# Performance work log

Hardware: AMD Instinct MI355X
Metric: run time of the kernel (lower is better)

The kernel has to match this reference:

```python
import jax, jax.numpy as jnp
import numpy as np


def setup_inputs() -> dict:
    key = jax.random.key(0)
    evecs = jax.random.normal(key, (4, 1, 1024, 16), dtype=jnp.float32)
    return {"evecs": evecs}


def reference(evecs):
    # Original wraps everything in torch.set_grad_enabled(False) -> block grads.
    evecs = jax.lax.stop_gradient(evecs)
    B, C, N, K = evecs.shape
    # For each level lvl, the torch loop computes X[..., :lvl+1] @ X[..., :lvl+1]^T,
    # i.e. the cumulative sum over k of rank-1 outer products e_k e_k^T.
    # outers[b, k, c, n, m] = evecs[b, c, n, k] * evecs[b, c, m, k]
    outers = jnp.einsum('bcnk,bcmk->bkcnm', evecs, evecs)
    cube = jnp.cumsum(outers, axis=1)          # running low-rank approximations
    # torch.cat(lras, dim=1): level-major then channel -> [B, K*C, N, N]
    return cube.reshape(B, K * C, N, N)
```

## Files before the change

kernel.cpp:

```cpp
#include <hip/hip_runtime.h>


#define BB 4
#define NN 1024
#define KK 16
#define ROWS 8

__global__ __launch_bounds__(256) void ExpandEvecs_75780402970966_kernel(
    const float* __restrict__ ev,
    float* __restrict__ out)
{
    const int tid = threadIdx.x;
    const int m0  = tid << 2;
    const int grp = blockIdx.x & 127;
    const int b   = blockIdx.x >> 7;
    const int n0  = grp * ROWS;

    const float* eb = ev + (size_t)b * NN * KK;

    float acc[ROWS][4];
#pragma unroll
    for (int r = 0; r < ROWS; ++r)
#pragma unroll
        for (int v = 0; v < 4; ++v) acc[r][v] = 0.0f;

    const size_t kplane = (size_t)NN * NN;
    const size_t obase  = (size_t)b * KK * kplane + (size_t)n0 * NN + (size_t)m0;

#pragma unroll
    for (int kb = 0; kb < KK / 4; ++kb) {
        float4 em4[4];
#pragma unroll
        for (int v = 0; v < 4; ++v)
            em4[v] = *(const float4*)(eb + (size_t)(m0 + v) * KK + kb * 4);

        float4 en4[ROWS];
#pragma unroll
        for (int r = 0; r < ROWS; ++r)
            en4[r] = *(const float4*)(eb + (size_t)(n0 + r) * KK + kb * 4);

#pragma unroll
        for (int kk = 0; kk < 4; ++kk) {
            const int k = kb * 4 + kk;
            float* outk = out + obase + (size_t)k * kplane;
#pragma unroll
            for (int r = 0; r < ROWS; ++r) {
                const float enk = ((const float*)&en4[r])[kk];
#pragma unroll
                for (int v = 0; v < 4; ++v)
                    acc[r][v] = fmaf(((const float*)&em4[v])[kk], enk, acc[r][v]);
                *(float4*)(outk + (size_t)r * NN) =
                    make_float4(acc[r][0], acc[r][1], acc[r][2], acc[r][3]);
            }
        }
    }
}

extern "C" void kernel_launch(void* const* d_in, const int* in_sizes, int n_in,
                              void* d_out, int out_size, void* d_ws, size_t ws_size,
                              hipStream_t stream) {
    const float* ev = (const float*)d_in[0];
    float* out = (float*)d_out;

    const int grid = BB * (NN / ROWS);
    ExpandEvecs_75780402970966_kernel<<<grid, 256, 0, stream>>>(ev, out);
}
```

Baseline: 257.0 us.

## Transpose evecs into workspace and emit one output row per block

Adds a pre-pass kernel that transposes evecs to a k-major layout in the workspace, so each thread can load its four m-columns per k as one coalesced float4. The main kernel now gives each block a single n row across all 16 levels and builds the cumulative outer product in registers before storing. The grid grows from 512 to 4096 blocks, and per-thread loads and register pressure drop. This costs an extra tiny kernel launch, plus a fallback path that transposes in registers when no workspace is available.

```diff
diff --git a/kernel.cpp b/kernel.cpp
--- a/kernel.cpp
+++ b/kernel.cpp
@@ -4,56 +4,75 @@
 #define BB 4
 #define NN 1024
 #define KK 16
-#define ROWS 8
 
+__global__ __launch_bounds__(256) void ExpandEvecs_75780402970966_evT(
+    const float* __restrict__ ev,
+    float* __restrict__ evT)
+{
+    const int b  = blockIdx.x >> 2;
+    const int mc = blockIdx.x & 3;
+    const int m  = mc * 256 + threadIdx.x;
+    const float* src = ev + (size_t)(b * NN + m) * KK;
+    float* dst = evT + (size_t)b * KK * NN + m;
+#pragma unroll
+    for (int k = 0; k < KK; ++k)
+        dst[(size_t)k * NN] = src[k];
+}
+
+template <bool TRANS>
 __global__ __launch_bounds__(256) void ExpandEvecs_75780402970966_kernel(
     const float* __restrict__ ev,
+    const float* __restrict__ evT,
     float* __restrict__ out)
 {
     const int tid = threadIdx.x;
     const int m0  = tid << 2;
-    const int grp = blockIdx.x & 127;
-    const int b   = blockIdx.x >> 7;
-    const int n0  = grp * ROWS;
+    const int n   = blockIdx.x & (NN - 1);
+    const int b   = blockIdx.x >> 10;
 
-    const float* eb = ev + (size_t)b * NN * KK;
+    const float* __restrict__ en = ev + (size_t)(b * NN + n) * KK;
 
-    float acc[ROWS][4];
+    float4 v[KK];
+    if (TRANS) {
+        const float* __restrict__ eT = evT + (size_t)b * KK * NN + m0;
 #pragma unroll
-    for (int r = 0; r < ROWS; ++r)
+        for (int k = 0; k < KK; ++k)
+            v[k] = *(const float4*)(eT + (size_t)k * NN);
+    } else {
+        float4 f[16];
+        const float* base = ev + ((size_t)b * NN + m0) * KK;
 #pragma unroll
-        for (int v = 0; v < 4; ++v) acc[r][v] = 0.0f;
+        for (int i = 0; i < 16; ++i)
+            f[i] = *(const float4*)(base + i * 4);
+#pragma unroll
+        for (int k = 0; k < KK; ++k) {
+            float4 t;
+            t.x = ((const float*)&f[0  + (k >> 2)])[k & 3];
+            t.y = ((const float*)&f[4  + (k >> 2)])[k & 3];
+            t.z = ((const float*)&f[8  + (k >> 2)])[k & 3];
+            t.w = ((const float*)&f[12 + (k >> 2)])[k & 3];
+            v[k] = t;
+        }
+    }
+
+    {
+        const float e0 = en[0];
+        v[0].x *= e0; v[0].y *= e0; v[0].z *= e0; v[0].w *= e0;
+    }
+#pragma unroll
+    for (int k = 1; k < KK; ++k) {
+        const float ek = en[k];
+        v[k].x = fmaf(v[k].x, ek, v[k - 1].x);
+        v[k].y = fmaf(v[k].y, ek, v[k - 1].y);
+        v[k].z = fmaf(v[k].z, ek, v[k - 1].z);
+        v[k].w = fmaf(v[k].w, ek, v[k - 1].w);
+    }
 
     const size_t kplane = (size_t)NN * NN;
-    const size_t obase  = (size_t)b * KK * kplane + (size_t)n0 * NN + (size_t)m0;
-
+    float* ob = out + (size_t)b * KK * kplane + (size_t)n * NN + m0;
 #pragma unroll
-    for (int kb = 0; kb < KK / 4; ++kb) {
-        float4 em4[4];
-#pragma unroll
-        for (int v = 0; v < 4; ++v)
-            em4[v] = *(const float4*)(eb + (size_t)(m0 + v) * KK + kb * 4);
-
-        float4 en4[ROWS];
-#pragma unroll
-        for (int r = 0; r < ROWS; ++r)
-            en4[r] = *(const float4*)(eb + (size_t)(n0 + r) * KK + kb * 4);
-
-#pragma unroll
-        for (int kk = 0; kk < 4; ++kk) {
-            const int k = kb * 4 + kk;
-            float* outk = out + obase + (size_t)k * kplane;
-#pragma unroll
-            for (int r = 0; r < ROWS; ++r) {
-                const float enk = ((const float*)&en4[r])[kk];
-#pragma unroll
-                for (int v = 0; v < 4; ++v)
-                    acc[r][v] = fmaf(((const float*)&em4[v])[kk], enk, acc[r][v]);
-                *(float4*)(outk + (size_t)r * NN) =
-                    make_float4(acc[r][0], acc[r][1], acc[r][2], acc[r][3]);
-            }
-        }
-    }
+    for (int k = 0; k < KK; ++k)
+        *(float4*)(ob + (size_t)k * kplane) = v[k];
 }
 
 extern "C" void kernel_launch(void* const* d_in, const int* in_sizes, int n_in,
@@ -62,6 +81,14 @@
     const float* ev = (const float*)d_in[0];
     float* out = (float*)d_out;
 
-    const int grid = BB * (NN / ROWS);
-    ExpandEvecs_75780402970966_kernel<<<grid, 256, 0, stream>>>(ev, out);
+    const size_t evT_bytes = (size_t)BB * KK * NN * sizeof(float);
+    if (ws_size >= evT_bytes && d_ws != nullptr) {
+        float* evT = (float*)d_ws;
+        ExpandEvecs_75780402970966_evT<<<BB * 4, 256, 0, stream>>>(ev, evT);
+        ExpandEvecs_75780402970966_kernel<true>
+            <<<BB * NN, 256, 0, stream>>>(ev, evT, out);
+    } else {
+        ExpandEvecs_75780402970966_kernel<false>
+            <<<BB * NN, 256, 0, stream>>>(ev, nullptr, out);
+    }
 }
```

Result: slower. 264.5 us (+2.9%).
